# Optimization experiments

Measured on AMD Instinct MI355X. Metric: run time of the kernel, lower is better.

The kernel has to match this reference:

```python
import jax, jax.numpy as jnp
import numpy as np

D_MODEL = 128
NUM_HEADS = 4
HEAD_DIM = D_MODEL // NUM_HEADS


def setup_inputs() -> dict:
    key = jax.random.key(0)
    k1, k2, k3, k4, k5 = jax.random.split(key, 5)
    B, T = 8, 2048
    x = jax.random.normal(k1, (B, T, D_MODEL), dtype=jnp.float32)
    s_in = 1.0 / np.sqrt(D_MODEL)
    W_qkv = jax.random.normal(k2, (D_MODEL, 3 * D_MODEL), dtype=jnp.float32) * s_in
    b_qkv = jnp.zeros((3 * D_MODEL,), dtype=jnp.float32)
    W_out = jax.random.normal(k3, (D_MODEL, D_MODEL), dtype=jnp.float32) * s_in
    b_out = jnp.zeros((D_MODEL,), dtype=jnp.float32)
    return {"x": x, "W_qkv": W_qkv, "b_qkv": b_qkv, "W_out": W_out, "b_out": b_out}


def reference(x, W_qkv, b_qkv, W_out, b_out):
    B, T, C = x.shape
    qkv = x @ W_qkv + b_qkv  # [B, T, 3C]
    q, k, v = jnp.split(qkv, 3, axis=-1)
    # [B, H, T, Dh]
    q = q.reshape(B, T, NUM_HEADS, HEAD_DIM).transpose(0, 2, 1, 3)
    k = k.reshape(B, T, NUM_HEADS, HEAD_DIM).transpose(0, 2, 1, 3)
    v = v.reshape(B, T, NUM_HEADS, HEAD_DIM).transpose(0, 2, 1, 3)
    scale = 1.0 / np.sqrt(HEAD_DIM).astype(np.float32)
    scores = jnp.einsum('bhtd,bhsd->bhts', q, k) * scale  # [B, H, T, T]
    causal = jnp.tril(jnp.ones((T, T), dtype=bool))
    scores = jnp.where(causal, scores, jnp.float32(-1e9))
    attn = jax.nn.softmax(scores, axis=-1)
    out = jnp.einsum('bhts,bhsd->bhtd', attn, v)  # [B, H, T, Dh]
    out = out.transpose(0, 2, 1, 3).reshape(B, T, C)
    return out @ W_out + b_out
```

## Files before the change

### kernel.cpp

```cpp
#include <hip/hip_runtime.h>
#include <hip/hip_bf16.h>
#include <math.h>

#define B_  8
#define T_  2048
#define C_  128
#define H_  4
#define DH_ 32
#define BH_ 32
#define NTOK 16384
#define QSCALE_ 0.25503486f


typedef __attribute__((ext_vector_type(8))) __bf16 bfrag;
typedef __attribute__((ext_vector_type(4))) float f32x4;
typedef __attribute__((ext_vector_type(16))) float f32x16;
typedef __attribute__((ext_vector_type(2))) unsigned int u32x2;
typedef __attribute__((ext_vector_type(4))) unsigned int u32x4;

__device__ __forceinline__ unsigned int pack2bf(float a, float b) {
    unsigned int ua = __float_as_uint(a);
    unsigned int ub = __float_as_uint(b);
    ua += 0x7fffu + ((ua >> 16) & 1u);
    ub += 0x7fffu + ((ub >> 16) & 1u);
    return (ua >> 16) | (ub & 0xffff0000u);
}

__device__ __forceinline__ unsigned int cvtpk_bf16(float lo, float hi) {
    unsigned int r;
    asm("v_cvt_pk_bf16_f32 %0, %1, %2" : "=v"(r) : "v"(lo), "v"(hi));
    return r;
}

__device__ __forceinline__ float fast_exp2(float x) {
    float r;
    asm("v_exp_f32 %0, %1" : "=v"(r) : "v"(x));
    return r;
}

__global__ __launch_bounds__(256)
void qkv_fused(const float* __restrict__ x, const float* __restrict__ Wqkv,
               const float* __restrict__ bqkv,
               __hip_bfloat16* __restrict__ Qf, __hip_bfloat16* __restrict__ Kf,
               __hip_bfloat16* __restrict__ Vf) {
    __shared__ __hip_bfloat16 Wl[24 * 4 * 64 * 8];
    const int tid = threadIdx.x;

    unsigned* Wlu = (unsigned*)Wl;
#pragma unroll 4
    for (int j = 0; j < 96; ++j) {
        const int i = j * 256 + tid;
        const int kk = i / 384;
        const int n  = i - kk * 384;
        const float lo = Wqkv[(2 * kk) * 384 + n];
        const float hi = Wqkv[(2 * kk + 1) * 384 + n];
        const int k = 2 * kk;
        const int nb = n >> 4, qi_ = n & 15;
        const int ks = k >> 5, grp_ = (k >> 3) & 3, off = k & 7;
        Wlu[(((nb * 4 + ks) * 64) + grp_ * 16 + qi_) * 4 + (off >> 1)] = cvtpk_bf16(lo, hi);
    }
    __syncthreads();

    const int w = tid >> 6, lane = tid & 63;
    const int qi = lane & 15, grp = lane >> 4;
    const int mbase = blockIdx.x * 64 + w * 16;

    const float* xrow = x + (size_t)(mbase + qi) * 128;
    bfrag xf[4];
#pragma unroll
    for (int ks = 0; ks < 4; ++ks) {
        const float4 a = *(const float4*)(xrow + ks * 32 + grp * 8);
        const float4 b = *(const float4*)(xrow + ks * 32 + grp * 8 + 4);
        u32x4 pk;
        pk.x = cvtpk_bf16(a.x, a.y);
        pk.y = cvtpk_bf16(a.z, a.w);
        pk.z = cvtpk_bf16(b.x, b.y);
        pk.w = cvtpk_bf16(b.z, b.w);
        xf[ks] = __builtin_bit_cast(bfrag, pk);
    }

    const long bb = mbase >> 11;
    const long tloc = mbase & 2047;
    const f32x4 zero = {0.f, 0.f, 0.f, 0.f};

#pragma unroll
    for (int nb = 0; nb < 24; ++nb) {
        f32x4 a = zero;
#pragma unroll
        for (int ks = 0; ks < 4; ++ks) {
            const bfrag wf = *(const bfrag*)&Wl[((nb * 4 + ks) * 64 + lane) * 8];
            if (nb < 16) a = __builtin_amdgcn_mfma_f32_16x16x32_bf16(wf, xf[ks], a, 0, 0, 0);
            else         a = __builtin_amdgcn_mfma_f32_16x16x32_bf16(xf[ks], wf, a, 0, 0, 0);
        }
        if (nb < 16) {
            const int c0 = nb * 16 + grp * 4;
            const float4 bias = *(const float4*)&bqkv[c0];
            const int local = c0 & 127;
            const int h = local >> 5, d0 = local & 31;
            __hip_bfloat16* dst = (nb < 8) ? Qf : Kf;
            const float sc = (nb < 8) ? QSCALE_ : 1.f;
            const long t = tloc + qi;
            const long bh = bb * H_ + h;
            const long blk = (bh * 64 + (t >> 5)) * 2 + (d0 >> 4);
            const int lanei = (int)(t & 31) + ((d0 & 15) >> 3) * 32;
            u32x2 pw;
            pw.x = pack2bf((a[0] + bias.x) * sc, (a[1] + bias.y) * sc);
            pw.y = pack2bf((a[2] + bias.z) * sc, (a[3] + bias.w) * sc);
            *(u32x2*)&dst[blk * 512 + lanei * 8 + (d0 & 7)] = pw;
        } else {
            const int c = nb * 16 + qi;
            const int local = c - 256;
            const int h = local >> 5, d = local & 31;
            const float bias = bqkv[c];
            const long t0 = tloc + grp * 4;
            const long bh = bb * H_ + h;
            const int s0 = (int)(t0 & 31);
            const long blk = (bh * 64 + (t0 >> 5)) * 2 + (s0 >> 4);
            const int lanei = d + ((s0 & 15) >> 3) * 32;
            u32x2 pw;
            pw.x = pack2bf(a[0] + bias, a[1] + bias);
            pw.y = pack2bf(a[2] + bias, a[3] + bias);
            *(u32x2*)&Vf[blk * 512 + lanei * 8 + (s0 & 7)] = pw;
        }
    }
}

__global__ __launch_bounds__(512, 4)
void attn_out(const __hip_bfloat16* __restrict__ Qf,
              const __hip_bfloat16* __restrict__ Kf,
              const __hip_bfloat16* __restrict__ Vf,
              const float* __restrict__ Wout,
              const float* __restrict__ bout, float* __restrict__ out) {
    __shared__ float csm[4][64][17];
    __shared__ unsigned int Osm[32][68];
    __shared__ __hip_bfloat16 Wo[32 * 64 * 8];

    const int lin = blockIdx.x;
    int b, c;
    if (lin < 256) { b = lin & 7; c = 63 - (lin >> 3); }
    else { const int m = lin - 256; b = m & 7; c = m >> 3; }

    {
        unsigned* Wou = (unsigned*)Wo;
#pragma unroll
        for (int j = 0; j < 16; ++j) {
            const int i = j * 512 + threadIdx.x;
            const int kk = i >> 7;
            const int n  = i & 127;
            const float lo = Wout[(2 * kk) * 128 + n];
            const float hi = Wout[(2 * kk + 1) * 128 + n];
            const int k = 2 * kk;
            const int hh = n >> 5, qn = n & 31;
            const int ks = k >> 4, hib = (k >> 3) & 1, off = k & 7;
            Wou[(((hh * 8 + ks) * 64) + hib * 32 + qn) * 4 + (off >> 1)] = cvtpk_bf16(lo, hi);
        }
    }

    const int w    = threadIdx.x >> 6;
    const int h    = w & 3;
    const int e    = w >> 2;
    const int lane = threadIdx.x & 63;
    const int ql   = lane & 31;
    const int hi   = lane >> 5;
    const int hi4  = hi * 4;

    const int bh = b * H_ + h;
    const int q  = c * 32 + ql;

    const __hip_bfloat16* Qp = Qf + (size_t)bh * 64 * 1024;
    const __hip_bfloat16* Kp = Kf + (size_t)bh * 64 * 1024;
    const __hip_bfloat16* Vp = Vf + (size_t)bh * 64 * 1024;

    const bfrag qf0 = *(const bfrag*)(Qp + (c * 2 + 0) * 512 + lane * 8);
    const bfrag qf1 = *(const bfrag*)(Qp + (c * 2 + 1) * 512 + lane * 8);

    f32x16 o;
#pragma unroll
    for (int r = 0; r < 16; ++r) o[r] = 0.f;
    float l = 0.f;

    auto ldK = [&](int u, bfrag& k0, bfrag& k1, bfrag& v0, bfrag& v1) {
        k0 = *(const bfrag*)(Kp + (u * 2 + 0) * 512 + lane * 8);
        k1 = *(const bfrag*)(Kp + (u * 2 + 1) * 512 + lane * 8);
        v0 = *(const bfrag*)(Vp + (u * 2 + 0) * 512 + lane * 8);
        v1 = *(const bfrag*)(Vp + (u * 2 + 1) * 512 + lane * 8);
    };

    auto proc = [&](const bfrag& kf0, const bfrag& kf1, const bfrag& vf0,
                    const bfrag& vf1, int sbase, bool band) {
        f32x16 s;
#pragma unroll
        for (int r = 0; r < 16; ++r) s[r] = 0.f;
        s = __builtin_amdgcn_mfma_f32_32x32x16_bf16(kf0, qf0, s, 0, 0, 0);
        s = __builtin_amdgcn_mfma_f32_32x32x16_bf16(kf1, qf1, s, 0, 0, 0);
        if (band) {
#pragma unroll
            for (int r = 0; r < 16; ++r) {
                const int srow = sbase + (r & 3) + 8 * (r >> 2) + hi4;
                if (srow > q) s[r] = -INFINITY;
            }
        }
#pragma unroll
        for (int r = 0; r < 16; ++r) { s[r] = fast_exp2(s[r]); l += s[r]; }
        u32x4 w0, w1;
        {
            unsigned a0 = cvtpk_bf16(s[0], s[1]);
            unsigned a1 = cvtpk_bf16(s[2], s[3]);
            unsigned a2 = cvtpk_bf16(s[4], s[5]);
            unsigned a3 = cvtpk_bf16(s[6], s[7]);
            auto r02 = __builtin_amdgcn_permlane32_swap((int)a0, (int)a2, false, false);
            auto r13 = __builtin_amdgcn_permlane32_swap((int)a1, (int)a3, false, false);
            w0.x = (unsigned)r02[0]; w0.y = (unsigned)r13[0];
            w0.z = (unsigned)r02[1]; w0.w = (unsigned)r13[1];
        }
        {
            unsigned a0 = cvtpk_bf16(s[8],  s[9]);
            unsigned a1 = cvtpk_bf16(s[10], s[11]);
            unsigned a2 = cvtpk_bf16(s[12], s[13]);
            unsigned a3 = cvtpk_bf16(s[14], s[15]);
            auto r02 = __builtin_amdgcn_permlane32_swap((int)a0, (int)a2, false, false);
            auto r13 = __builtin_amdgcn_permlane32_swap((int)a1, (int)a3, false, false);
            w1.x = (unsigned)r02[0]; w1.y = (unsigned)r13[0];
            w1.z = (unsigned)r02[1]; w1.w = (unsigned)r13[1];
        }
        o = __builtin_amdgcn_mfma_f32_32x32x16_bf16(
                vf0, __builtin_bit_cast(bfrag, w0), o, 0, 0, 0);
        o = __builtin_amdgcn_mfma_f32_32x32x16_bf16(
                vf1, __builtin_bit_cast(bfrag, w1), o, 0, 0, 0);
    };

    if (e <= c) {
        bfrag ck0, ck1, cv0, cv1, nk0, nk1, nv0, nv1;
        ldK(e, ck0, ck1, cv0, cv1);
        for (int u = e; u <= c; u += 2) {
            if (u + 2 <= c) ldK(u + 2, nk0, nk1, nv0, nv1);
            proc(ck0, ck1, cv0, cv1, u * 32, u == c);
            ck0 = nk0; ck1 = nk1; cv0 = nv0; cv1 = nv1;
        }
    }

    l += __shfl_xor(l, 32);

    if (e == 1) {
        float* my = &csm[h][lane][0];
        f32x4 t0 = {o[0], o[1], o[2], o[3]};
        f32x4 t1 = {o[4], o[5], o[6], o[7]};
        f32x4 t2 = {o[8], o[9], o[10], o[11]};
        f32x4 t3 = {o[12], o[13], o[14], o[15]};
        *(f32x4*)(my + 0) = t0;  *(f32x4*)(my + 4) = t1;
        *(f32x4*)(my + 8) = t2;  *(f32x4*)(my + 12) = t3;
        my[16] = l;
    }
    __syncthreads();
    if (e == 0) {
        const float* pr = &csm[h][lane][0];
#pragma unroll
        for (int r = 0; r < 16; ++r) o[r] += pr[r];
        l += pr[16];
        const float rl = 1.f / l;
#pragma unroll
        for (int pi = 0; pi < 8; ++pi) {
            const int r = pi * 2;
            const int n = (r & 3) + 8 * (r >> 2) + hi4;
            Osm[ql][(h * 32 + n) >> 1] = cvtpk_bf16(o[r] * rl, o[r + 1] * rl);
        }
    }
    __syncthreads();

    if (e == 0) {
        f32x16 acc;
#pragma unroll
        for (int r = 0; r < 16; ++r) acc[r] = 0.f;
#pragma unroll
        for (int ks = 0; ks < 8; ++ks) {
            const bfrag wf = *(const bfrag*)&Wo[((h * 8 + ks) * 64 + lane) * 8];
            const u32x4 ofu = *(const u32x4*)&Osm[ql][ks * 8 + hi4];
            acc = __builtin_amdgcn_mfma_f32_32x32x16_bf16(
                      wf, __builtin_bit_cast(bfrag, ofu), acc, 0, 0, 0);
        }
        float* orow = out + ((size_t)b * T_ + c * 32 + ql) * 128 + h * 32;
#pragma unroll
        for (int pi = 0; pi < 8; ++pi) {
            const int r = pi * 2;
            const int n = (r & 3) + 8 * (r >> 2) + hi4;
            const float2 bb2 = *(const float2*)&bout[h * 32 + n];
            float2 ov;
            ov.x = acc[r] + bb2.x;
            ov.y = acc[r + 1] + bb2.y;
            *(float2*)&orow[n] = ov;
        }
    }
}

extern "C" void kernel_launch(void* const* d_in, const int* in_sizes, int n_in,
                              void* d_out, int out_size, void* d_ws, size_t ws_size,
                              hipStream_t stream) {
    const float* x    = (const float*)d_in[0];
    const float* Wqkv = (const float*)d_in[1];
    const float* bqkv = (const float*)d_in[2];
    const float* Wout = (const float*)d_in[3];
    const float* bout = (const float*)d_in[4];
    float* out = (float*)d_out;

    const size_t per = (size_t)BH_ * T_ * DH_;
    __hip_bfloat16* Qf = (__hip_bfloat16*)d_ws;
    __hip_bfloat16* Kf = Qf + per;
    __hip_bfloat16* Vf = Kf + per;

    qkv_fused<<<256, 256, 0, stream>>>(x, Wqkv, bqkv, Qf, Kf, Vf);

    attn_out<<<512, 512, 0, stream>>>(Qf, Kf, Vf, Wout, bout, out);
}
```

Before: 41.23 us.

## Split QKV projection across Q/K/V blocks and ping-pong attention K/V buffers

```diff
diff --git a/kernel.cpp b/kernel.cpp
--- a/kernel.cpp
+++ b/kernel.cpp
@@ -39,31 +39,35 @@
 }
 
 __global__ __launch_bounds__(256)
-void qkv_fused(const float* __restrict__ x, const float* __restrict__ Wqkv,
-               const float* __restrict__ bqkv,
-               __hip_bfloat16* __restrict__ Qf, __hip_bfloat16* __restrict__ Kf,
-               __hip_bfloat16* __restrict__ Vf) {
-    __shared__ __hip_bfloat16 Wl[24 * 4 * 64 * 8];
-    const int tid = threadIdx.x;
+void qkv_part(const float* __restrict__ x, const float* __restrict__ Wqkv,
+              const float* __restrict__ bqkv,
+              __hip_bfloat16* __restrict__ Qf, __hip_bfloat16* __restrict__ Kf,
+              __hip_bfloat16* __restrict__ Vf) {
+    __shared__ __hip_bfloat16 Wl[8 * 4 * 64 * 8];
+    const int bid  = blockIdx.x;
+    const int kind = bid >> 8;
+    const int tb   = bid & 255;
+    const int tid  = threadIdx.x;
+    const int cbase = kind << 7;
 
     unsigned* Wlu = (unsigned*)Wl;
-#pragma unroll 4
-    for (int j = 0; j < 96; ++j) {
-        const int i = j * 256 + tid;
-        const int kk = i / 384;
-        const int n  = i - kk * 384;
-        const float lo = Wqkv[(2 * kk) * 384 + n];
-        const float hi = Wqkv[(2 * kk + 1) * 384 + n];
+#pragma unroll
+    for (int j = 0; j < 32; ++j) {
+        const int i  = j * 256 + tid;
+        const int kk = i >> 7;
+        const int nl = i & 127;
+        const float lo = Wqkv[(2 * kk) * 384 + cbase + nl];
+        const float hi = Wqkv[(2 * kk + 1) * 384 + cbase + nl];
         const int k = 2 * kk;
-        const int nb = n >> 4, qi_ = n & 15;
-        const int ks = k >> 5, grp_ = (k >> 3) & 3, off = k & 7;
-        Wlu[(((nb * 4 + ks) * 64) + grp_ * 16 + qi_) * 4 + (off >> 1)] = cvtpk_bf16(lo, hi);
+        const int nb = nl >> 4, qi_ = nl & 15;
+        const int ks = k >> 5, grp_ = (k >> 3) & 3;
+        Wlu[(((nb * 4 + ks) * 64) + grp_ * 16 + qi_) * 4 + ((k & 7) >> 1)] = cvtpk_bf16(lo, hi);
     }
     __syncthreads();
 
     const int w = tid >> 6, lane = tid & 63;
     const int qi = lane & 15, grp = lane >> 4;
-    const int mbase = blockIdx.x * 64 + w * 16;
+    const int mbase = tb * 64 + w * 16;
 
     const float* xrow = x + (size_t)(mbase + qi) * 128;
     bfrag xf[4];
@@ -84,21 +88,22 @@
     const f32x4 zero = {0.f, 0.f, 0.f, 0.f};
 
 #pragma unroll
-    for (int nb = 0; nb < 24; ++nb) {
+    for (int nbl = 0; nbl < 8; ++nbl) {
+        const int nb = kind * 8 + nbl;
         f32x4 a = zero;
 #pragma unroll
         for (int ks = 0; ks < 4; ++ks) {
-            const bfrag wf = *(const bfrag*)&Wl[((nb * 4 + ks) * 64 + lane) * 8];
-            if (nb < 16) a = __builtin_amdgcn_mfma_f32_16x16x32_bf16(wf, xf[ks], a, 0, 0, 0);
-            else         a = __builtin_amdgcn_mfma_f32_16x16x32_bf16(xf[ks], wf, a, 0, 0, 0);
-        }
-        if (nb < 16) {
+            const bfrag wf = *(const bfrag*)&Wl[((nbl * 4 + ks) * 64 + lane) * 8];
+            if (kind < 2) a = __builtin_amdgcn_mfma_f32_16x16x32_bf16(wf, xf[ks], a, 0, 0, 0);
+            else          a = __builtin_amdgcn_mfma_f32_16x16x32_bf16(xf[ks], wf, a, 0, 0, 0);
+        }
+        if (kind < 2) {
             const int c0 = nb * 16 + grp * 4;
             const float4 bias = *(const float4*)&bqkv[c0];
             const int local = c0 & 127;
             const int h = local >> 5, d0 = local & 31;
-            __hip_bfloat16* dst = (nb < 8) ? Qf : Kf;
-            const float sc = (nb < 8) ? QSCALE_ : 1.f;
+            __hip_bfloat16* dst = (kind == 0) ? Qf : Kf;
+            const float sc = (kind == 0) ? QSCALE_ : 1.f;
             const long t = tloc + qi;
             const long bh = bb * H_ + h;
             const long blk = (bh * 64 + (t >> 5)) * 2 + (d0 >> 4);
@@ -151,8 +156,8 @@
             const float hi = Wout[(2 * kk + 1) * 128 + n];
             const int k = 2 * kk;
             const int hh = n >> 5, qn = n & 31;
-            const int ks = k >> 4, hib = (k >> 3) & 1, off = k & 7;
-            Wou[(((hh * 8 + ks) * 64) + hib * 32 + qn) * 4 + (off >> 1)] = cvtpk_bf16(lo, hi);
+            const int ks = k >> 4, hib = (k >> 3) & 1;
+            Wou[(((hh * 8 + ks) * 64) + hib * 32 + qn) * 4 + ((k & 7) >> 1)] = cvtpk_bf16(lo, hi);
         }
     }
 
@@ -174,9 +179,9 @@
     const bfrag qf0 = *(const bfrag*)(Qp + (c * 2 + 0) * 512 + lane * 8);
     const bfrag qf1 = *(const bfrag*)(Qp + (c * 2 + 1) * 512 + lane * 8);
 
-    f32x16 o;
-#pragma unroll
-    for (int r = 0; r < 16; ++r) o[r] = 0.f;
+    f32x16 o, z16;
+#pragma unroll
+    for (int r = 0; r < 16; ++r) { o[r] = 0.f; z16[r] = 0.f; }
     float l = 0.f;
 
     auto ldK = [&](int u, bfrag& k0, bfrag& k1, bfrag& v0, bfrag& v1) {
@@ -188,10 +193,7 @@
 
     auto proc = [&](const bfrag& kf0, const bfrag& kf1, const bfrag& vf0,
                     const bfrag& vf1, int sbase, bool band) {
-        f32x16 s;
-#pragma unroll
-        for (int r = 0; r < 16; ++r) s[r] = 0.f;
-        s = __builtin_amdgcn_mfma_f32_32x32x16_bf16(kf0, qf0, s, 0, 0, 0);
+        f32x16 s = __builtin_amdgcn_mfma_f32_32x32x16_bf16(kf0, qf0, z16, 0, 0, 0);
         s = __builtin_amdgcn_mfma_f32_32x32x16_bf16(kf1, qf1, s, 0, 0, 0);
         if (band) {
 #pragma unroll
@@ -201,7 +203,14 @@
             }
         }
 #pragma unroll
-        for (int r = 0; r < 16; ++r) { s[r] = fast_exp2(s[r]); l += s[r]; }
+        for (int r = 0; r < 16; ++r) s[r] = fast_exp2(s[r]);
+        {
+            float t0 = (s[0] + s[1]) + (s[2] + s[3]);
+            float t1 = (s[4] + s[5]) + (s[6] + s[7]);
+            float t2 = (s[8] + s[9]) + (s[10] + s[11]);
+            float t3 = (s[12] + s[13]) + (s[14] + s[15]);
+            l += (t0 + t1) + (t2 + t3);
+        }
         u32x4 w0, w1;
         {
             unsigned a0 = cvtpk_bf16(s[0], s[1]);
@@ -230,12 +239,18 @@
     };
 
     if (e <= c) {
-        bfrag ck0, ck1, cv0, cv1, nk0, nk1, nv0, nv1;
-        ldK(e, ck0, ck1, cv0, cv1);
-        for (int u = e; u <= c; u += 2) {
-            if (u + 2 <= c) ldK(u + 2, nk0, nk1, nv0, nv1);
-            proc(ck0, ck1, cv0, cv1, u * 32, u == c);
-            ck0 = nk0; ck1 = nk1; cv0 = nv0; cv1 = nv1;
+        bfrag ak0, ak1, av0, av1, bk0, bk1, bv0, bv1;
+        int u = e;
+        ldK(u, ak0, ak1, av0, av1);
+        while (true) {
+            if (u + 2 <= c) ldK(u + 2, bk0, bk1, bv0, bv1);
+            proc(ak0, ak1, av0, av1, u * 32, u == c);
+            u += 2;
+            if (u > c) break;
+            if (u + 2 <= c) ldK(u + 2, ak0, ak1, av0, av1);
+            proc(bk0, bk1, bv0, bv1, u * 32, u == c);
+            u += 2;
+            if (u > c) break;
         }
     }
 
@@ -307,7 +322,7 @@
     __hip_bfloat16* Kf = Qf + per;
     __hip_bfloat16* Vf = Kf + per;
 
-    qkv_fused<<<256, 256, 0, stream>>>(x, Wqkv, bqkv, Qf, Kf, Vf);
+    qkv_part<<<768, 256, 0, stream>>>(x, Wqkv, bqkv, Qf, Kf, Vf);
 
     attn_out<<<512, 512, 0, stream>>>(Qf, Kf, Vf, Wout, bout, out);
 }
```

Measured after the change: 37.52 us (median of 2 runs). 9.0% less time.
